# Performance work log

Measured on AMD Instinct MI355X. Metric: run time of the kernel, lower is better.

## Reference

```python
import jax, jax.numpy as jnp
import numpy as np
import math


def setup_inputs() -> dict:
    key = jax.random.key(0)
    k1, k2, k3, k4 = jax.random.split(key, 4)
    b, h, T, dk = 1, 8, 4096, 64
    BS = 64
    T_q = 2048
    num_blocks = T // BS
    q = jax.random.normal(k1, (b, h, T_q, dk), dtype=jnp.float32)
    k = jax.random.normal(k2, (b, h, T, dk), dtype=jnp.float32)
    v = jax.random.normal(k3, (b, h, T, dk), dtype=jnp.float32)
    top2_idx = jax.random.randint(k4, (b, h, T_q, 2), 0, num_blocks, dtype=jnp.int32)
    return {"q": q, "k": k, "v": v, "BS": BS, "top2_idx": top2_idx}


def reference(q, k, v, BS, top2_idx):
    b, h, T, dk = k.shape
    num_blocks = T // BS
    T_q = top2_idx.shape[2]
    # [b,h,num_blocks,BS,dk]
    k_blocks = k.reshape(b, h, num_blocks, BS, dk)
    v_blocks = v.reshape(b, h, num_blocks, BS, dk)
    # gather 2 blocks per query: flat idx [b,h,T_q*2] -> select along block axis
    flat_idx = top2_idx.reshape(b, h, T_q * 2)[..., None, None]  # [b,h,2*T_q,1,1]
    k_sel = jnp.take_along_axis(k_blocks, flat_idx, axis=2).reshape(b, h, T_q, 2 * BS, dk)
    v_sel = jnp.take_along_axis(v_blocks, flat_idx, axis=2).reshape(b, h, T_q, 2 * BS, dk)
    # per-query attention over its 2*BS gathered keys
    score = jnp.einsum("bhqd,bhqkd->bhqk", q, k_sel) / math.sqrt(dk)
    score = jax.nn.softmax(score, axis=-1)
    out = jnp.einsum("bhqk,bhqkd->bhqd", score, v_sel)
    return out
```

## Files before the change

kernel.cpp:

```cpp
#include <hip/hip_runtime.h>


#define NH      8
#define TQ      2048
#define TKV     4096
#define DK      64
#define BSZ     64
#define NB      (TKV / BSZ)
#define NQ_TOT  (NH * TQ)
#define NENT    (NQ_TOT * 2)
#define NBUCKET (NH * NB)
#define SSPLIT  2
#define CAP     256

#define WS_LIST_B    4096
#define WS_PART_B    528384
#define WS_NEEDED    (WS_PART_B + (size_t)NENT * 68 * 4)

typedef __attribute__((ext_vector_type(8))) short bf16x8;
typedef __attribute__((ext_vector_type(4))) float f32x4;

__device__ __forceinline__ short f2bf(float x) {
    union { float f; unsigned u; } c; c.f = x;
    unsigned r = c.u + 0x7fffu + ((c.u >> 16) & 1u);
    return (short)(r >> 16);
}

__device__ __forceinline__ bf16x8 pack_bf16x8(float4 a, float4 b) {
    bf16x8 r;
    r[0] = f2bf(a.x); r[1] = f2bf(a.y); r[2] = f2bf(a.z); r[3] = f2bf(a.w);
    r[4] = f2bf(b.x); r[5] = f2bf(b.y); r[6] = f2bf(b.z); r[7] = f2bf(b.w);
    return r;
}

__global__ __launch_bounds__(NBUCKET) void zero_cursor_kernel(int* __restrict__ cursor)
{
    cursor[threadIdx.x] = 0;
}

__global__ __launch_bounds__(256) void scatter_kernel(
    const int* __restrict__ top2, int* __restrict__ cursor, int* __restrict__ list)
{
    const int e = blockIdx.x * 256 + threadIdx.x;
    const int qi = e >> 1;
    const int blk = top2[e] & (NB - 1);
    const int b = ((qi >> 11) << 6) | blk;
    int pos = atomicAdd(cursor + b, 1);
    pos = (pos < 0) ? 0 : (pos >= CAP ? CAP - 1 : pos);
    list[b * CAP + pos] = e;
}

#define KSTR 72
#define VSTR 78

__global__ __launch_bounds__(256, 2) void bucket_kernel(
    const float* __restrict__ q,
    const float* __restrict__ k,
    const float* __restrict__ v,
    const int*   __restrict__ cursor,
    const int*   __restrict__ list,
    float*       __restrict__ partials)
{
    __shared__ __align__(16) short K_lds[BSZ * KSTR];
    __shared__ __align__(16) short V_lds[BSZ * VSTR];
    __shared__ __align__(16) short P_lds[4][16 * 72];

    const int bucket  = blockIdx.x & (NBUCKET - 1);
    const int subtile = blockIdx.x >> 9;
    const int wave = threadIdx.x >> 6;
    const int lane = threadIdx.x & 63;
    const int W    = subtile * 4 + wave;

    const int start = bucket * CAP;
    int nq = cursor[bucket];
    nq = (nq > CAP) ? CAP : nq;
    const int ntiles = (nq + 15) >> 4;
    if (ntiles <= subtile * 4) return;

    const int h    = bucket >> 6;
    const int blk  = bucket & (NB - 1);
    const int n16  = lane & 15;
    const int quad = lane >> 4;

    const float* kb = k + ((size_t)h * TKV + (size_t)blk * BSZ) * DK;
    const float* vb = v + ((size_t)h * TKV + (size_t)blk * BSZ) * DK;

    {
        const int row = threadIdx.x >> 2;
        const int seg = threadIdx.x & 3;
        const float* kp = kb + row * DK + seg * 16;
        const float* vp = vb + row * DK + seg * 16;
        short* kd = &K_lds[row * KSTR + seg * 16];
        short* vd = &V_lds[row * VSTR + seg * 16];
#pragma unroll
        for (int c = 0; c < 4; ++c) {
            const float4 a = *(const float4*)(kp + c * 4);
            kd[c * 4 + 0] = f2bf(a.x); kd[c * 4 + 1] = f2bf(a.y);
            kd[c * 4 + 2] = f2bf(a.z); kd[c * 4 + 3] = f2bf(a.w);
            const float4 b = *(const float4*)(vp + c * 4);
            vd[c * 4 + 0] = f2bf(b.x); vd[c * 4 + 1] = f2bf(b.y);
            vd[c * 4 + 2] = f2bf(b.z); vd[c * 4 + 3] = f2bf(b.w);
        }
    }
    __syncthreads();
    if (W >= ntiles) return;

    bf16x8 kf[4][2];
#pragma unroll
    for (int kt = 0; kt < 4; ++kt)
#pragma unroll
        for (int ks = 0; ks < 2; ++ks)
            kf[kt][ks] = *(const bf16x8*)&K_lds[(kt * 16 + n16) * KSTR + ks * 32 + quad * 8];

    bf16x8 vf[4][2];
#pragma unroll
    for (int dt = 0; dt < 4; ++dt)
#pragma unroll
        for (int ks = 0; ks < 2; ++ks) {
            bf16x8 t;
#pragma unroll
            for (int jj = 0; jj < 8; ++jj)
                t[jj] = V_lds[(ks * 32 + quad * 8 + jj) * VSTR + dt * 16 + n16];
            vf[dt][ks] = t;
        }

    short* pl = &P_lds[wave][0];

    for (int t = W; t < ntiles; t += 4 * SSPLIT) {
        const int tbase = start + t * 16;

        const int em_idx = (t * 16 + n16 < nq) ? (tbase + n16) : start;
        const int qi = list[em_idx] >> 1;
        bf16x8 qf[2];
#pragma unroll
        for (int ks = 0; ks < 2; ++ks) {
            const float* p = q + (size_t)qi * DK + ks * 32 + quad * 8;
            float4 lo = *(const float4*)p, hi = *(const float4*)(p + 4);
            lo.x *= 0.125f; lo.y *= 0.125f; lo.z *= 0.125f; lo.w *= 0.125f;
            hi.x *= 0.125f; hi.y *= 0.125f; hi.z *= 0.125f; hi.w *= 0.125f;
            qf[ks] = pack_bf16x8(lo, hi);
        }

        f32x4 acc[4];
#pragma unroll
        for (int kt = 0; kt < 4; ++kt) {
            f32x4 a = {0.f, 0.f, 0.f, 0.f};
            a = __builtin_amdgcn_mfma_f32_16x16x32_bf16(qf[0], kf[kt][0], a, 0, 0, 0);
            a = __builtin_amdgcn_mfma_f32_16x16x32_bf16(qf[1], kf[kt][1], a, 0, 0, 0);
            acc[kt] = a;
        }

        float m4[4], l4[4], P[4][4];
#pragma unroll
        for (int r = 0; r < 4; ++r) {
            float mx = fmaxf(fmaxf(acc[0][r], acc[1][r]), fmaxf(acc[2][r], acc[3][r]));
            mx = fmaxf(mx, __shfl_xor(mx, 1));
            mx = fmaxf(mx, __shfl_xor(mx, 2));
            mx = fmaxf(mx, __shfl_xor(mx, 4));
            mx = fmaxf(mx, __shfl_xor(mx, 8));
            float s = 0.f;
#pragma unroll
            for (int kt = 0; kt < 4; ++kt) { P[kt][r] = __expf(acc[kt][r] - mx); s += P[kt][r]; }
            s += __shfl_xor(s, 1);
            s += __shfl_xor(s, 2);
            s += __shfl_xor(s, 4);
            s += __shfl_xor(s, 8);
            m4[r] = mx; l4[r] = s;
        }

#pragma unroll
        for (int r = 0; r < 4; ++r)
#pragma unroll
            for (int kt = 0; kt < 4; ++kt)
                pl[(quad * 4 + r) * 72 + kt * 16 + n16] = f2bf(P[kt][r]);

        bf16x8 pf[2];
#pragma unroll
        for (int ks = 0; ks < 2; ++ks)
            pf[ks] = *(const bf16x8*)&pl[n16 * 72 + ks * 32 + quad * 8];

        f32x4 oacc[4];
#pragma unroll
        for (int dt = 0; dt < 4; ++dt) {
            f32x4 a = {0.f, 0.f, 0.f, 0.f};
            a = __builtin_amdgcn_mfma_f32_16x16x32_bf16(pf[0], vf[dt][0], a, 0, 0, 0);
            a = __builtin_amdgcn_mfma_f32_16x16x32_bf16(pf[1], vf[dt][1], a, 0, 0, 0);
            oacc[dt] = a;
        }

#pragma unroll
        for (int r = 0; r < 4; ++r) {
            const int row = t * 16 + quad * 4 + r;
            if (row < nq) {
                const int e = list[tbase + quad * 4 + r];
                float* pp = partials + (size_t)e * 68;
#pragma unroll
                for (int dt = 0; dt < 4; ++dt)
                    pp[dt * 16 + n16] = oacc[dt][r];
                if (n16 == 0) pp[64] = m4[r];
                if (n16 == 1) pp[65] = l4[r];
            }
        }
    }
}

__global__ __launch_bounds__(256) void combine_kernel(
    const float* __restrict__ partials, float* __restrict__ out)
{
    const int t  = blockIdx.x * 256 + threadIdx.x;
    const int qi = t >> 4;
    const int dc = t & 15;
    const float* p0 = partials + (size_t)(qi * 2) * 68;
    const float* p1 = p0 + 68;
    const float m0 = p0[64], l0 = p0[65];
    const float m1 = p1[64], l1 = p1[65];
    const float m  = fmaxf(m0, m1);
    const float a0 = __expf(m0 - m), a1 = __expf(m1 - m);
    const float inv = 1.0f / (a0 * l0 + a1 * l1);
    const float4 o0 = *(const float4*)(p0 + dc * 4);
    const float4 o1 = *(const float4*)(p1 + dc * 4);
    float4 o;
    o.x = (o0.x * a0 + o1.x * a1) * inv;
    o.y = (o0.y * a0 + o1.y * a1) * inv;
    o.z = (o0.z * a0 + o1.z * a1) * inv;
    o.w = (o0.w * a0 + o1.w * a1) * inv;
    *(float4*)(out + (size_t)qi * DK + dc * 4) = o;
}

__global__ __launch_bounds__(256) void blockattn_fallback(
    const float* __restrict__ q, const float* __restrict__ k,
    const float* __restrict__ v, const int* __restrict__ top2,
    float* __restrict__ out)
{
    const int wave = threadIdx.x >> 6;
    const int lane = threadIdx.x & 63;
    const int qidx = (blockIdx.x << 2) + wave;
    const int bh   = qidx >> 11;
    const int g    = lane >> 4;
    const int dc   = lane & 15;

    const int2 idx = *(const int2*)(top2 + (size_t)qidx * 2);
    const size_t bh_off = (size_t)bh * (TKV * DK);
    const int off = g * DK + dc * 4;

    const float* kb0 = k + bh_off + (size_t)idx.x * (BSZ * DK) + off;
    const float* kb1 = k + bh_off + (size_t)idx.y * (BSZ * DK) + off;
    const float* vb0 = v + bh_off + (size_t)idx.x * (BSZ * DK) + off;
    const float* vb1 = v + bh_off + (size_t)idx.y * (BSZ * DK) + off;
    const float4 qf = *(const float4*)(q + (size_t)qidx * DK + dc * 4);

    float sc[32];
#pragma unroll
    for (int i = 0; i < 16; ++i) {
        const float4 a = *(const float4*)(kb0 + i * 256);
        float p = a.x*qf.x + a.y*qf.y + a.z*qf.z + a.w*qf.w;
        p += __shfl_xor(p,1); p += __shfl_xor(p,2); p += __shfl_xor(p,4); p += __shfl_xor(p,8);
        sc[i] = p * 0.125f;
    }
#pragma unroll
    for (int i = 0; i < 16; ++i) {
        const float4 a = *(const float4*)(kb1 + i * 256);
        float p = a.x*qf.x + a.y*qf.y + a.z*qf.z + a.w*qf.w;
        p += __shfl_xor(p,1); p += __shfl_xor(p,2); p += __shfl_xor(p,4); p += __shfl_xor(p,8);
        sc[16+i] = p * 0.125f;
    }
    float m = sc[0];
#pragma unroll
    for (int i = 1; i < 32; ++i) m = fmaxf(m, sc[i]);
    m = fmaxf(m, __shfl_xor(m,16)); m = fmaxf(m, __shfl_xor(m,32));
    float sum = 0.f;
#pragma unroll
    for (int i = 0; i < 32; ++i) { sc[i] = __expf(sc[i]-m); sum += sc[i]; }
    sum += __shfl_xor(sum,16); sum += __shfl_xor(sum,32);
    const float inv = 1.0f / sum;

    float4 acc = make_float4(0.f,0.f,0.f,0.f);
#pragma unroll
    for (int i = 0; i < 16; ++i) {
        const float4 a = *(const float4*)(vb0 + i * 256);
        acc.x += a.x*sc[i]; acc.y += a.y*sc[i]; acc.z += a.z*sc[i]; acc.w += a.w*sc[i];
    }
#pragma unroll
    for (int i = 0; i < 16; ++i) {
        const float4 a = *(const float4*)(vb1 + i * 256);
        acc.x += a.x*sc[16+i]; acc.y += a.y*sc[16+i]; acc.z += a.z*sc[16+i]; acc.w += a.w*sc[16+i];
    }
    acc.x += __shfl_xor(acc.x,16); acc.y += __shfl_xor(acc.y,16);
    acc.z += __shfl_xor(acc.z,16); acc.w += __shfl_xor(acc.w,16);
    acc.x += __shfl_xor(acc.x,32); acc.y += __shfl_xor(acc.y,32);
    acc.z += __shfl_xor(acc.z,32); acc.w += __shfl_xor(acc.w,32);

    if (g == 0) {
        float4 o;
        o.x = acc.x*inv; o.y = acc.y*inv; o.z = acc.z*inv; o.w = acc.w*inv;
        *(float4*)(out + (size_t)qidx * DK + dc * 4) = o;
    }
}

extern "C" void kernel_launch(void* const* d_in, const int* in_sizes, int n_in,
                              void* d_out, int out_size, void* d_ws, size_t ws_size,
                              hipStream_t stream) {
    const float* q    = (const float*)d_in[0];
    const float* k    = (const float*)d_in[1];
    const float* v    = (const float*)d_in[2];
    const int*   top2 = (const int*)d_in[4];
    float*       out  = (float*)d_out;

    if (ws_size < WS_NEEDED) {
        dim3 grid(NQ_TOT / 4), block(256);
        hipLaunchKernelGGL(blockattn_fallback, grid, block, 0, stream, q, k, v, top2, out);
        return;
    }

    char* ws = (char*)d_ws;
    int* cursor  = (int*)ws;
    int* list    = (int*)(ws + WS_LIST_B);
    float* parts = (float*)(ws + WS_PART_B);

    hipLaunchKernelGGL(zero_cursor_kernel, dim3(1),          dim3(NBUCKET), 0, stream, cursor);
    hipLaunchKernelGGL(scatter_kernel,     dim3(NENT / 256), dim3(256), 0, stream, top2, cursor, list);
    hipLaunchKernelGGL(bucket_kernel,      dim3(NBUCKET * SSPLIT), dim3(256), 0, stream, q, k, v, cursor, list, parts);
    hipLaunchKernelGGL(combine_kernel,     dim3(NQ_TOT * 16 / 256), dim3(256), 0, stream, parts, out);
}
```

Measured before the change: 92.23 us.

## Build per-bucket query lists in-kernel via prefix scan, dropping scatter kernels

The separate zero-cursor and atomic scatter kernels are removed. Each bucket block now scans its head's whole top2 array (4096 entries), counts the matches with a wave prefix scan, and writes a deterministic query list into LDS. This removes two kernel launches, the global atomics and the global list reads. In exchange every block (1024 of them) redundantly reads 16KB of indices and runs the scan before any compute, and the two __syncthreads add latency.

```diff
diff --git a/kernel.cpp b/kernel.cpp
--- a/kernel.cpp
+++ b/kernel.cpp
@@ -13,9 +13,7 @@
 #define SSPLIT  2
 #define CAP     256
 
-#define WS_LIST_B    4096
-#define WS_PART_B    528384
-#define WS_NEEDED    (WS_PART_B + (size_t)NENT * 68 * 4)
+#define WS_NEEDED    ((size_t)NENT * 68 * 4)
 
 typedef __attribute__((ext_vector_type(8))) short bf16x8;
 typedef __attribute__((ext_vector_type(4))) float f32x4;
@@ -33,23 +31,6 @@
     return r;
 }
 
-__global__ __launch_bounds__(NBUCKET) void zero_cursor_kernel(int* __restrict__ cursor)
-{
-    cursor[threadIdx.x] = 0;
-}
-
-__global__ __launch_bounds__(256) void scatter_kernel(
-    const int* __restrict__ top2, int* __restrict__ cursor, int* __restrict__ list)
-{
-    const int e = blockIdx.x * 256 + threadIdx.x;
-    const int qi = e >> 1;
-    const int blk = top2[e] & (NB - 1);
-    const int b = ((qi >> 11) << 6) | blk;
-    int pos = atomicAdd(cursor + b, 1);
-    pos = (pos < 0) ? 0 : (pos >= CAP ? CAP - 1 : pos);
-    list[b * CAP + pos] = e;
-}
-
 #define KSTR 72
 #define VSTR 78
 
@@ -57,13 +38,14 @@
     const float* __restrict__ q,
     const float* __restrict__ k,
     const float* __restrict__ v,
-    const int*   __restrict__ cursor,
-    const int*   __restrict__ list,
+    const int*   __restrict__ top2,
     float*       __restrict__ partials)
 {
     __shared__ __align__(16) short K_lds[BSZ * KSTR];
     __shared__ __align__(16) short V_lds[BSZ * VSTR];
     __shared__ __align__(16) short P_lds[4][16 * 72];
+    __shared__ int lds_list[CAP];
+    __shared__ int wave_tot[4];
 
     const int bucket  = blockIdx.x & (NBUCKET - 1);
     const int subtile = blockIdx.x >> 9;
@@ -71,14 +53,44 @@
     const int lane = threadIdx.x & 63;
     const int W    = subtile * 4 + wave;
 
-    const int start = bucket * CAP;
-    int nq = cursor[bucket];
+    const int h    = bucket >> 6;
+    const int blk  = bucket & (NB - 1);
+
+    const int* th = top2 + h * (TQ * 2);
+    int cnt = 0;
+#pragma unroll
+    for (int rep = 0; rep < (TQ * 2) / 256; ++rep) {
+        if ((th[rep * 256 + threadIdx.x] & (NB - 1)) == blk) ++cnt;
+    }
+    int pre = cnt;
+#pragma unroll
+    for (int off = 1; off < 64; off <<= 1) {
+        const int nb = __shfl_up(pre, off);
+        if (lane >= off) pre += nb;
+    }
+    if (lane == 63) wave_tot[wave] = pre;
+    __syncthreads();
+    int wbase = 0;
+#pragma unroll
+    for (int wv = 0; wv < 4; ++wv) if (wv < wave) wbase += wave_tot[wv];
+    int nq = wave_tot[0] + wave_tot[1] + wave_tot[2] + wave_tot[3];
     nq = (nq > CAP) ? CAP : nq;
+    {
+        int p = wbase + pre - cnt;
+#pragma unroll
+        for (int rep = 0; rep < (TQ * 2) / 256; ++rep) {
+            const int i = rep * 256 + threadIdx.x;
+            if ((th[i] & (NB - 1)) == blk) {
+                if (p < CAP) lds_list[p] = h * (TQ * 2) + i;
+                ++p;
+            }
+        }
+    }
+    __syncthreads();
+
     const int ntiles = (nq + 15) >> 4;
     if (ntiles <= subtile * 4) return;
 
-    const int h    = bucket >> 6;
-    const int blk  = bucket & (NB - 1);
     const int n16  = lane & 15;
     const int quad = lane >> 4;
 
@@ -127,10 +139,10 @@
     short* pl = &P_lds[wave][0];
 
     for (int t = W; t < ntiles; t += 4 * SSPLIT) {
-        const int tbase = start + t * 16;
-
-        const int em_idx = (t * 16 + n16 < nq) ? (tbase + n16) : start;
-        const int qi = list[em_idx] >> 1;
+        const int tbase = t * 16;
+
+        const int em_idx = (tbase + n16 < nq) ? (tbase + n16) : 0;
+        const int qi = lds_list[em_idx] >> 1;
         bf16x8 qf[2];
 #pragma unroll
         for (int ks = 0; ks < 2; ++ks) {
@@ -190,9 +202,9 @@
 
 #pragma unroll
         for (int r = 0; r < 4; ++r) {
-            const int row = t * 16 + quad * 4 + r;
+            const int row = tbase + quad * 4 + r;
             if (row < nq) {
-                const int e = list[tbase + quad * 4 + r];
+                const int e = lds_list[row];
                 float* pp = partials + (size_t)e * 68;
 #pragma unroll
                 for (int dt = 0; dt < 4; ++dt)
@@ -312,13 +324,10 @@
         return;
     }
 
-    char* ws = (char*)d_ws;
-    int* cursor  = (int*)ws;
-    int* list    = (int*)(ws + WS_LIST_B);
-    float* parts = (float*)(ws + WS_PART_B);
-
-    hipLaunchKernelGGL(zero_cursor_kernel, dim3(1),          dim3(NBUCKET), 0, stream, cursor);
-    hipLaunchKernelGGL(scatter_kernel,     dim3(NENT / 256), dim3(256), 0, stream, top2, cursor, list);
-    hipLaunchKernelGGL(bucket_kernel,      dim3(NBUCKET * SSPLIT), dim3(256), 0, stream, q, k, v, cursor, list, parts);
-    hipLaunchKernelGGL(combine_kernel,     dim3(NQ_TOT * 16 / 256), dim3(256), 0, stream, parts, out);
-}
+    float* parts = (float*)d_ws;
+
+    hipLaunchKernelGGL(bucket_kernel,  dim3(NBUCKET * SSPLIT), dim3(256), 0, stream,
+                       q, k, v, top2, parts);
+    hipLaunchKernelGGL(combine_kernel, dim3(NQ_TOT * 16 / 256), dim3(256), 0, stream,
+                       parts, out);
+}
```

Result: faster. 83.41 us, median of 2 (-9.6%).
